# Kernel tuning notes

Hardware: AMD Instinct MI355X
Metric: run time of the kernel (lower is better)

The kernel has to match this reference:

```python
import jax, jax.numpy as jnp
import numpy as np

N = 50000   # nodes
E = 800000  # edges
F = 256     # feature dim (in = hidden = out)
L = 3       # number_layers


def _arma_conv(x, src, dst, w, Wi, Wr, b):
    # GCN normalization without self loops (PyG ARMAConv default)
    deg = jax.ops.segment_sum(w, dst, num_segments=N)                 # [N]
    dinv = jnp.where(deg > 0, jax.lax.rsqrt(deg), 0.0)
    norm = dinv[src] * w * dinv[dst]                                   # [E]
    h = x @ Wi                                                         # [N, F]
    agg = jax.ops.segment_sum(norm[:, None] * h[src], dst, num_segments=N)  # [N, F]
    # root dropout is inactive in eval mode
    return jax.nn.relu(agg + x @ Wr + b)


def setup_inputs() -> dict:
    key = jax.random.key(0)
    ks = jax.random.split(key, 6)
    x = jax.random.normal(ks[0], (N, F), jnp.float32)
    edge_index = jax.random.randint(ks[1], (2, E), 0, N, jnp.int32)
    edge_attr = jax.random.uniform(ks[2], (E,), jnp.float32)
    s = 1.0 / np.sqrt(F)
    W_init = jax.random.normal(ks[3], (L, F, F), jnp.float32) * s
    W_root = jax.random.normal(ks[4], (L, F, F), jnp.float32) * s
    bias = jnp.zeros((L, F), jnp.float32)
    return dict(x=x, edge_index=edge_index, edge_attr=edge_attr,
                W_init=W_init, W_root=W_root, bias=bias)


def reference(x, edge_index, edge_attr, W_init, W_root, bias):
    src, dst = edge_index[0], edge_index[1]
    for i in range(L):  # fixed small layer count
        x = _arma_conv(x, src, dst, edge_attr, W_init[i], W_root[i], bias[i])
        # outer functional.relu is a no-op after the conv's internal ReLU;
        # dropout is inactive in eval mode.
    return x
```

## Files before the change

### kernel.cpp

```cpp
#include <hip/hip_runtime.h>
#include <hip/hip_bf16.h>

#define N_NODES 50000
#define N_EDGES 800000
#define FDIM 256
#define N_LAYERS 3

typedef __attribute__((ext_vector_type(8))) short bf16x8;
typedef __attribute__((ext_vector_type(4))) float f32x4;

__device__ inline unsigned short f2bf(float f) {
  unsigned int u = __float_as_uint(f);
  unsigned int r = u + 0x7FFFu + ((u >> 16) & 1u);
  return (unsigned short)(r >> 16);
}
__device__ inline float bf2f(unsigned short s) {
  return __uint_as_float(((unsigned int)s) << 16);
}
__device__ inline void split2(float f, unsigned short& h, unsigned short& l) {
  h = f2bf(f);
  l = f2bf(f - bf2f(h));
}

#define GLOAD16(g, l) __builtin_amdgcn_global_load_lds( \
    (const __attribute__((address_space(1))) void*)(g), \
    (__attribute__((address_space(3))) void*)(l), 16, 0, 0)


__global__ void deg_count_kernel(const int* __restrict__ dst,
                                 const float* __restrict__ w,
                                 float* __restrict__ deg,
                                 int* __restrict__ cnt, int E) {
  int e = blockIdx.x * blockDim.x + threadIdx.x;
  if (e < E) {
    int d = dst[e];
    atomicAdd(&deg[d], w[e]);
    atomicAdd(&cnt[d], 1);
  }
}

__global__ void dinv_kernel(const float* __restrict__ deg,
                            float* __restrict__ dinv, int n) {
  int i = blockIdx.x * blockDim.x + threadIdx.x;
  if (i < n) {
    float d = deg[i];
    dinv[i] = (d > 0.f) ? (1.f / sqrtf(d)) : 0.f;
  }
}

__global__ __launch_bounds__(1024)
void scan_kernel(const int* __restrict__ cnt, int* __restrict__ offs,
                 int* __restrict__ cursor, int n) {
  __shared__ int wsums[16];
  __shared__ int carry_s;
  int t = threadIdx.x;
  int lane = t & 63, wid = t >> 6;
  if (t == 0) carry_s = 0;
  __syncthreads();
  for (int base = 0; base < n; base += 1024) {
    int i = base + t;
    int v = (i < n) ? cnt[i] : 0;
    int incl = v;
    #pragma unroll
    for (int d = 1; d < 64; d <<= 1) {
      int tmp = __shfl_up(incl, d, 64);
      if (lane >= d) incl += tmp;
    }
    if (lane == 63) wsums[wid] = incl;
    __syncthreads();
    if (t == 0) {
      int s = carry_s;
      #pragma unroll
      for (int k = 0; k < 16; ++k) { int tt = wsums[k]; wsums[k] = s; s += tt; }
      carry_s = s;
    }
    __syncthreads();
    int excl = incl - v + wsums[wid];
    if (i < n) { offs[i] = excl; cursor[i] = excl; }
    __syncthreads();
  }
  if (t == 0) offs[n] = carry_s;
}

__global__ void scatter_kernel(const int* __restrict__ src,
                               const int* __restrict__ dst,
                               const float* __restrict__ w,
                               const float* __restrict__ dinv,
                               int* __restrict__ cursor,
                               int* __restrict__ src_s,
                               float* __restrict__ norm_s, int E) {
  int e = blockIdx.x * blockDim.x + threadIdx.x;
  if (e < E) {
    int s = src[e], d = dst[e];
    int pos = atomicAdd(&cursor[d], 1);
    src_s[pos] = s;
    norm_s[pos] = dinv[s] * w[e] * dinv[d];
  }
}

__global__ void split_kernel(const float* __restrict__ x,
                             unsigned short* __restrict__ xhi,
                             unsigned short* __restrict__ xlo, int n4) {
  int i = blockIdx.x * blockDim.x + threadIdx.x;
  if (i < n4) {
    float4 v = reinterpret_cast<const float4*>(x)[i];
    ushort4 h, l;
    split2(v.x, h.x, l.x);
    split2(v.y, h.y, l.y);
    split2(v.z, h.z, l.z);
    split2(v.w, h.w, l.w);
    reinterpret_cast<ushort4*>(xhi)[i] = h;
    reinterpret_cast<ushort4*>(xlo)[i] = l;
  }
}

__global__ __launch_bounds__(256)
void wsplit_kernel(const float* __restrict__ Wi_a,
                   const float* __restrict__ Wr_a,
                   unsigned short* __restrict__ wthi,
                   unsigned short* __restrict__ wtlo) {
  __shared__ float tile[32][33];
  int m6 = blockIdx.x >> 6;
  int tid = blockIdx.x & 63;
  int tk = (tid >> 3) * 32;
  int tn = (tid & 7) * 32;
  int layer = m6 >> 1;
  const float* W = ((m6 & 1) ? Wr_a : Wi_a) + (size_t)layer * FDIM * FDIM;
  int t = threadIdx.x;
  int lr = t >> 3;
  int lc = (t & 7) * 4;
  float4 v = *reinterpret_cast<const float4*>(W + (size_t)(tk + lr) * FDIM + tn + lc);
  tile[lr][lc + 0] = v.x; tile[lr][lc + 1] = v.y;
  tile[lr][lc + 2] = v.z; tile[lr][lc + 3] = v.w;
  __syncthreads();
  ushort4 h, l;
  split2(tile[lc + 0][lr], h.x, l.x);
  split2(tile[lc + 1][lr], h.y, l.y);
  split2(tile[lc + 2][lr], h.z, l.z);
  split2(tile[lc + 3][lr], h.w, l.w);
  size_t o = ((size_t)m6 * FDIM + tn + lr) * FDIM + tk + lc;
  *reinterpret_cast<ushort4*>(wthi + o) = h;
  *reinterpret_cast<ushort4*>(wtlo + o) = l;
}


__global__ __launch_bounds__(256)
void agg_kernel(const unsigned short* __restrict__ xh,
                const float* __restrict__ norm_s,
                const int* __restrict__ src_s,
                const int* __restrict__ offs,
                unsigned short* __restrict__ agh,
                unsigned short* __restrict__ agl, int n) {
  int node = blockIdx.x * 4 + (threadIdx.x >> 6);
  if (node >= n) return;
  int lane = threadIdx.x & 63;
  int beg = offs[node];
  int end = offs[node + 1];
  float a0 = 0.f, a1 = 0.f, a2 = 0.f, a3 = 0.f;
  int j = beg;
  for (; j + 4 <= end; j += 4) {
    int s0 = src_s[j], s1 = src_s[j + 1], s2 = src_s[j + 2], s3 = src_s[j + 3];
    float w0 = norm_s[j], w1 = norm_s[j + 1], w2 = norm_s[j + 2], w3 = norm_s[j + 3];
    ushort4 v0 = *reinterpret_cast<const ushort4*>(xh + (size_t)s0 * FDIM + lane * 4);
    ushort4 v1 = *reinterpret_cast<const ushort4*>(xh + (size_t)s1 * FDIM + lane * 4);
    ushort4 v2 = *reinterpret_cast<const ushort4*>(xh + (size_t)s2 * FDIM + lane * 4);
    ushort4 v3 = *reinterpret_cast<const ushort4*>(xh + (size_t)s3 * FDIM + lane * 4);
    a0 += w0 * bf2f(v0.x) + w1 * bf2f(v1.x) + w2 * bf2f(v2.x) + w3 * bf2f(v3.x);
    a1 += w0 * bf2f(v0.y) + w1 * bf2f(v1.y) + w2 * bf2f(v2.y) + w3 * bf2f(v3.y);
    a2 += w0 * bf2f(v0.z) + w1 * bf2f(v1.z) + w2 * bf2f(v2.z) + w3 * bf2f(v3.z);
    a3 += w0 * bf2f(v0.w) + w1 * bf2f(v1.w) + w2 * bf2f(v2.w) + w3 * bf2f(v3.w);
  }
  for (; j < end; ++j) {
    int s = src_s[j];
    float wv = norm_s[j];
    ushort4 v = *reinterpret_cast<const ushort4*>(xh + (size_t)s * FDIM + lane * 4);
    a0 += wv * bf2f(v.x); a1 += wv * bf2f(v.y);
    a2 += wv * bf2f(v.z); a3 += wv * bf2f(v.w);
  }
  ushort4 hh, ll;
  split2(a0, hh.x, ll.x);
  split2(a1, hh.y, ll.y);
  split2(a2, hh.z, ll.z);
  split2(a3, hh.w, ll.w);
  size_t base = (size_t)node * FDIM + lane * 4;
  *reinterpret_cast<ushort4*>(agh + base) = hh;
  *reinterpret_cast<ushort4*>(agl + base) = ll;
}


#define STAGE_TILE(TI, GPTR, ROWB, CLAMP)                                        \
  {                                                                              \
    int s0 = t;                                                                  \
    int rr = s0 >> 2;                                                            \
    int sl = (s0 & 3) ^ ((rr >> 1) & 3);                                         \
    int r2 = (ROWB) + rr; if (CLAMP && r2 >= M) r2 = M - 1;                      \
    GLOAD16((GPTR) + (size_t)r2 * FDIM + k0 + sl * 8, smem + (TI)*8192 + s0*16); \
    int s1 = t + 256;                                                            \
    rr = s1 >> 2;                                                                \
    sl = (s1 & 3) ^ ((rr >> 1) & 3);                                             \
    r2 = (ROWB) + rr; if (CLAMP && r2 >= M) r2 = M - 1;                          \
    GLOAD16((GPTR) + (size_t)r2 * FDIM + k0 + sl * 8, smem + (TI)*8192 + s1*16); \
  }

__global__ __launch_bounds__(256, 2)
void gemm_dual_kernel(const unsigned short* __restrict__ agh,
                      const unsigned short* __restrict__ agl,
                      const unsigned short* __restrict__ xh,
                      const unsigned short* __restrict__ xl,
                      const unsigned short* __restrict__ wih,
                      const unsigned short* __restrict__ wil,
                      const unsigned short* __restrict__ wrh,
                      const unsigned short* __restrict__ wrl,
                      const float* __restrict__ bias,
                      unsigned short* __restrict__ oh,
                      unsigned short* __restrict__ ol,
                      float* __restrict__ ofinal,
                      int writeFinal, int M) {
  __shared__ __align__(16) unsigned char smem[65536];
  const int t = threadIdx.x;
  const int lane = t & 63;
  const int w = t >> 6;
  const int rowBase = blockIdx.x * 128;
  const int nBase = blockIdx.y * 128;

  const int wm = (w >> 1) * 64;
  const int wn = (w & 1) * 64;

  f32x4 acc[4][4];
  #pragma unroll
  for (int i = 0; i < 4; ++i)
    #pragma unroll
    for (int j = 0; j < 4; ++j)
      acc[i][j] = (f32x4)(0.f);

  for (int k0 = 0; k0 < FDIM; k0 += 32) {
    STAGE_TILE(0, agh, rowBase, 1);
    STAGE_TILE(1, agl, rowBase, 1);
    STAGE_TILE(2, xh, rowBase, 1);
    STAGE_TILE(3, xl, rowBase, 1);
    STAGE_TILE(4, wih, nBase, 0);
    STAGE_TILE(5, wil, nBase, 0);
    STAGE_TILE(6, wrh, nBase, 0);
    STAGE_TILE(7, wrl, nBase, 0);
    __syncthreads();

    const int q = lane >> 4;
    bf16x8 fah[4], fal[4], fxh[4], fxl[4];
    #pragma unroll
    for (int i = 0; i < 4; ++i) {
      int R = wm + i * 16 + (lane & 15);
      int offA = R * 64 + ((q ^ ((R >> 1) & 3)) * 16);
      fah[i] = *reinterpret_cast<const bf16x8*>(smem + offA);
      fal[i] = *reinterpret_cast<const bf16x8*>(smem + 8192 + offA);
      fxh[i] = *reinterpret_cast<const bf16x8*>(smem + 16384 + offA);
      fxl[i] = *reinterpret_cast<const bf16x8*>(smem + 24576 + offA);
    }
    #pragma unroll
    for (int j = 0; j < 4; ++j) {
      int Rb = wn + j * 16 + (lane & 15);
      int offB = Rb * 64 + ((q ^ ((Rb >> 1) & 3)) * 16);
      bf16x8 bwih = *reinterpret_cast<const bf16x8*>(smem + 32768 + offB);
      bf16x8 bwil = *reinterpret_cast<const bf16x8*>(smem + 40960 + offB);
      bf16x8 bwrh = *reinterpret_cast<const bf16x8*>(smem + 49152 + offB);
      bf16x8 bwrl = *reinterpret_cast<const bf16x8*>(smem + 57344 + offB);
      #pragma unroll
      for (int i = 0; i < 4; ++i) {
        acc[i][j] = __builtin_amdgcn_mfma_f32_16x16x32_bf16(fal[i], bwih, acc[i][j], 0, 0, 0);
        acc[i][j] = __builtin_amdgcn_mfma_f32_16x16x32_bf16(fah[i], bwil, acc[i][j], 0, 0, 0);
        acc[i][j] = __builtin_amdgcn_mfma_f32_16x16x32_bf16(fah[i], bwih, acc[i][j], 0, 0, 0);
        acc[i][j] = __builtin_amdgcn_mfma_f32_16x16x32_bf16(fxl[i], bwrh, acc[i][j], 0, 0, 0);
        acc[i][j] = __builtin_amdgcn_mfma_f32_16x16x32_bf16(fxh[i], bwrl, acc[i][j], 0, 0, 0);
        acc[i][j] = __builtin_amdgcn_mfma_f32_16x16x32_bf16(fxh[i], bwrh, acc[i][j], 0, 0, 0);
      }
    }
    __syncthreads();
  }

  const int cr = lane & 15;
  const int r4 = (lane >> 4) * 4;
  #pragma unroll
  for (int i = 0; i < 4; ++i)
    #pragma unroll
    for (int j = 0; j < 4; ++j) {
      int col = nBase + wn + j * 16 + cr;
      float badd = bias[col];
      #pragma unroll
      for (int e = 0; e < 4; ++e) {
        int row = rowBase + wm + i * 16 + r4 + e;
        if (row < M) {
          float val = fmaxf(acc[i][j][e] + badd, 0.f);
          size_t o = (size_t)row * FDIM + col;
          if (writeFinal) {
            ofinal[o] = val;
          } else {
            unsigned short hh, ll;
            split2(val, hh, ll);
            oh[o] = hh;
            ol[o] = ll;
          }
        }
      }
    }
}


extern "C" void kernel_launch(void* const* d_in, const int* in_sizes, int n_in,
                              void* d_out, int out_size, void* d_ws, size_t ws_size,
                              hipStream_t stream) {
  (void)in_sizes; (void)n_in; (void)out_size; (void)ws_size;
  const float* x0   = (const float*)d_in[0];
  const int*   ei   = (const int*)d_in[1];
  const float* ea   = (const float*)d_in[2];
  const float* Wi_a = (const float*)d_in[3];
  const float* Wr_a = (const float*)d_in[4];
  const float* b_a  = (const float*)d_in[5];
  float* out = (float*)d_out;

  const int* src = ei;
  const int* dst = ei + N_EDGES;

  char* ws = (char*)d_ws;
  size_t off = 0;
  auto alloc = [&](size_t bytes) {
    char* p = ws + off;
    off += (bytes + 255) & ~(size_t)255;
    return p;
  };
  const size_t NF2 = (size_t)N_NODES * FDIM * 2;
  unsigned short* XAh = (unsigned short*)alloc(NF2);
  unsigned short* XAl = (unsigned short*)alloc(NF2);
  unsigned short* XBh = (unsigned short*)alloc(NF2);
  unsigned short* XBl = (unsigned short*)alloc(NF2);
  unsigned short* agh = (unsigned short*)alloc(NF2);
  unsigned short* agl = (unsigned short*)alloc(NF2);
  unsigned short* wthi = (unsigned short*)alloc((size_t)N_LAYERS * 2 * FDIM * FDIM * 2);
  unsigned short* wtlo = (unsigned short*)alloc((size_t)N_LAYERS * 2 * FDIM * FDIM * 2);
  float* deg    = (float*)alloc((size_t)N_NODES * 4);
  float* dinv   = (float*)alloc((size_t)N_NODES * 4);
  int*   cnt    = (int*)alloc((size_t)N_NODES * 4);
  int*   offs   = (int*)alloc((size_t)(N_NODES + 1) * 4);
  int*   cursor = (int*)alloc((size_t)N_NODES * 4);
  int*   src_s  = (int*)alloc((size_t)N_EDGES * 4);
  float* norm_s = (float*)alloc((size_t)N_EDGES * 4);

  hipMemsetAsync(deg, 0, (size_t)N_NODES * 4, stream);
  hipMemsetAsync(cnt, 0, (size_t)N_NODES * 4, stream);

  deg_count_kernel<<<(N_EDGES + 255) / 256, 256, 0, stream>>>(dst, ea, deg, cnt, N_EDGES);
  dinv_kernel<<<(N_NODES + 255) / 256, 256, 0, stream>>>(deg, dinv, N_NODES);
  scan_kernel<<<1, 1024, 0, stream>>>(cnt, offs, cursor, N_NODES);
  scatter_kernel<<<(N_EDGES + 255) / 256, 256, 0, stream>>>(src, dst, ea, dinv, cursor,
                                                            src_s, norm_s, N_EDGES);
  wsplit_kernel<<<6 * 64, 256, 0, stream>>>(Wi_a, Wr_a, wthi, wtlo);
  int n4 = N_NODES * FDIM / 4;
  split_kernel<<<(n4 + 255) / 256, 256, 0, stream>>>(x0, XAh, XAl, n4);

  const size_t WMAT = (size_t)FDIM * FDIM;
  dim3 ggrid((N_NODES + 127) / 128, 2);
  unsigned short* curh = XAh; unsigned short* curl = XAl;
  unsigned short* nxth = XBh; unsigned short* nxtl = XBl;
  for (int l = 0; l < N_LAYERS; ++l) {
    agg_kernel<<<(N_NODES + 3) / 4, 256, 0, stream>>>(curh, norm_s, src_s, offs,
                                                      agh, agl, N_NODES);
    int writeFinal = (l == N_LAYERS - 1) ? 1 : 0;
    gemm_dual_kernel<<<ggrid, 256, 0, stream>>>(
        agh, agl, curh, curl,
        wthi + (size_t)(l * 2) * WMAT, wtlo + (size_t)(l * 2) * WMAT,
        wthi + (size_t)(l * 2 + 1) * WMAT, wtlo + (size_t)(l * 2 + 1) * WMAT,
        b_a + (size_t)l * FDIM,
        nxth, nxtl, out, writeFinal, N_NODES);
    unsigned short* th = curh; unsigned short* tl = curl;
    curh = nxth; curl = nxtl; nxth = th; nxtl = tl;
  }
}
```

Before: 733.3 us.

## Parallelize CSR offset scan and overlap GEMM tile loads with MFMA compute

Replaces the single-block serial prefix scan over 50k node counts with a three-kernel block-sum, block-prefix and per-block offset scan, so the scan runs across many workgroups. In the dual GEMM, each k-step loads all A and B fragments from LDS into registers, waits and barriers, then issues the asynchronous global-to-LDS loads for the next k-slice before running the MFMAs, so global loads overlap compute in a single buffer. The grid is flattened so the two column tiles of the same row block get adjacent block IDs, which should improve L2 reuse of the A rows. This costs more registers for the B fragments and adds two kernel launches.

```diff
diff --git a/kernel.cpp b/kernel.cpp
--- a/kernel.cpp
+++ b/kernel.cpp
@@ -5,6 +5,7 @@
 #define N_EDGES 800000
 #define FDIM 256
 #define N_LAYERS 3
+#define NB_SCAN ((N_NODES + 255) / 256)
 
 typedef __attribute__((ext_vector_type(8))) short bf16x8;
 typedef __attribute__((ext_vector_type(4))) float f32x4;
@@ -48,38 +49,71 @@
   }
 }
 
-__global__ __launch_bounds__(1024)
-void scan_kernel(const int* __restrict__ cnt, int* __restrict__ offs,
-                 int* __restrict__ cursor, int n) {
-  __shared__ int wsums[16];
-  __shared__ int carry_s;
+__global__ __launch_bounds__(256)
+void blocksum_kernel(const int* __restrict__ cnt, int* __restrict__ bsum, int n) {
+  int b = blockIdx.x;
+  int t = threadIdx.x;
+  int i = b * 256 + t;
+  int v = (i < n) ? cnt[i] : 0;
+  #pragma unroll
+  for (int d = 1; d < 64; d <<= 1) v += __shfl_xor(v, d, 64);
+  __shared__ int ws[4];
+  if ((t & 63) == 0) ws[t >> 6] = v;
+  __syncthreads();
+  if (t == 0) bsum[b] = ws[0] + ws[1] + ws[2] + ws[3];
+}
+
+__global__ __launch_bounds__(256)
+void scanb_kernel(const int* __restrict__ bsum, int* __restrict__ bpre,
+                  int* __restrict__ offs_end) {
   int t = threadIdx.x;
   int lane = t & 63, wid = t >> 6;
-  if (t == 0) carry_s = 0;
-  __syncthreads();
-  for (int base = 0; base < n; base += 1024) {
-    int i = base + t;
-    int v = (i < n) ? cnt[i] : 0;
-    int incl = v;
-    #pragma unroll
-    for (int d = 1; d < 64; d <<= 1) {
-      int tmp = __shfl_up(incl, d, 64);
-      if (lane >= d) incl += tmp;
-    }
-    if (lane == 63) wsums[wid] = incl;
-    __syncthreads();
-    if (t == 0) {
-      int s = carry_s;
-      #pragma unroll
-      for (int k = 0; k < 16; ++k) { int tt = wsums[k]; wsums[k] = s; s += tt; }
-      carry_s = s;
-    }
-    __syncthreads();
-    int excl = incl - v + wsums[wid];
-    if (i < n) { offs[i] = excl; cursor[i] = excl; }
-    __syncthreads();
-  }
-  if (t == 0) offs[n] = carry_s;
+  int v = (t < NB_SCAN) ? bsum[t] : 0;
+  int incl = v;
+  #pragma unroll
+  for (int d = 1; d < 64; d <<= 1) {
+    int tmp = __shfl_up(incl, d, 64);
+    if (lane >= d) incl += tmp;
+  }
+  __shared__ int wsum[4];
+  if (lane == 63) wsum[wid] = incl;
+  __syncthreads();
+  if (t == 0) {
+    int s = 0;
+    #pragma unroll
+    for (int k = 0; k < 4; ++k) { int tt = wsum[k]; wsum[k] = s; s += tt; }
+  }
+  __syncthreads();
+  int excl = incl - v + wsum[wid];
+  if (t < NB_SCAN) bpre[t] = excl;
+  if (t == NB_SCAN - 1) *offs_end = excl + v;
+}
+
+__global__ __launch_bounds__(256)
+void offs_kernel(const int* __restrict__ cnt, const int* __restrict__ bpre,
+                 int* __restrict__ offs, int* __restrict__ cursor, int n) {
+  int b = blockIdx.x;
+  int t = threadIdx.x;
+  int lane = t & 63, wid = t >> 6;
+  int i = b * 256 + t;
+  int v = (i < n) ? cnt[i] : 0;
+  int incl = v;
+  #pragma unroll
+  for (int d = 1; d < 64; d <<= 1) {
+    int tmp = __shfl_up(incl, d, 64);
+    if (lane >= d) incl += tmp;
+  }
+  __shared__ int wsum[4];
+  if (lane == 63) wsum[wid] = incl;
+  __syncthreads();
+  if (t == 0) {
+    int s = 0;
+    #pragma unroll
+    for (int k = 0; k < 4; ++k) { int tt = wsum[k]; wsum[k] = s; s += tt; }
+  }
+  __syncthreads();
+  int excl = incl - v + wsum[wid] + bpre[b];
+  if (i < n) { offs[i] = excl; cursor[i] = excl; }
 }
 
 __global__ void scatter_kernel(const int* __restrict__ src,
@@ -188,19 +222,31 @@
 }
 
 
-#define STAGE_TILE(TI, GPTR, ROWB, CLAMP)                                        \
-  {                                                                              \
-    int s0 = t;                                                                  \
-    int rr = s0 >> 2;                                                            \
-    int sl = (s0 & 3) ^ ((rr >> 1) & 3);                                         \
-    int r2 = (ROWB) + rr; if (CLAMP && r2 >= M) r2 = M - 1;                      \
-    GLOAD16((GPTR) + (size_t)r2 * FDIM + k0 + sl * 8, smem + (TI)*8192 + s0*16); \
-    int s1 = t + 256;                                                            \
-    rr = s1 >> 2;                                                                \
-    sl = (s1 & 3) ^ ((rr >> 1) & 3);                                             \
-    r2 = (ROWB) + rr; if (CLAMP && r2 >= M) r2 = M - 1;                          \
-    GLOAD16((GPTR) + (size_t)r2 * FDIM + k0 + sl * 8, smem + (TI)*8192 + s1*16); \
-  }
+#define STAGE_TILE(TI, GPTR, ROWB, CLAMP, K0)                                     \
+  {                                                                               \
+    int s0_ = t;                                                                  \
+    int rr_ = s0_ >> 2;                                                           \
+    int sl_ = (s0_ & 3) ^ ((rr_ >> 1) & 3);                                       \
+    int r2_ = (ROWB) + rr_; if (CLAMP && r2_ >= M) r2_ = M - 1;                   \
+    GLOAD16((GPTR) + (size_t)r2_ * FDIM + (K0) + sl_ * 8,                         \
+            smem + (TI) * 8192 + s0_ * 16);                                       \
+    int s1_ = t + 256;                                                            \
+    rr_ = s1_ >> 2;                                                               \
+    sl_ = (s1_ & 3) ^ ((rr_ >> 1) & 3);                                           \
+    r2_ = (ROWB) + rr_; if (CLAMP && r2_ >= M) r2_ = M - 1;                       \
+    GLOAD16((GPTR) + (size_t)r2_ * FDIM + (K0) + sl_ * 8,                         \
+            smem + (TI) * 8192 + s1_ * 16);                                       \
+  }
+
+#define STAGE_ALL(K0)                      \
+  STAGE_TILE(0, agh, rowBase, 1, K0);      \
+  STAGE_TILE(1, agl, rowBase, 1, K0);      \
+  STAGE_TILE(2, xh, rowBase, 1, K0);       \
+  STAGE_TILE(3, xl, rowBase, 1, K0);       \
+  STAGE_TILE(4, wih, nBase, 0, K0);        \
+  STAGE_TILE(5, wil, nBase, 0, K0);        \
+  STAGE_TILE(6, wrh, nBase, 0, K0);        \
+  STAGE_TILE(7, wrl, nBase, 0, K0);
 
 __global__ __launch_bounds__(256, 2)
 void gemm_dual_kernel(const unsigned short* __restrict__ agh,
@@ -220,8 +266,9 @@
   const int t = threadIdx.x;
   const int lane = t & 63;
   const int w = t >> 6;
-  const int rowBase = blockIdx.x * 128;
-  const int nBase = blockIdx.y * 128;
+  const int bid = blockIdx.x;
+  const int rowBase = (bid >> 1) * 128;
+  const int nBase = (bid & 1) * 128;
 
   const int wm = (w >> 1) * 64;
   const int wn = (w & 1) * 64;
@@ -233,19 +280,14 @@
     for (int j = 0; j < 4; ++j)
       acc[i][j] = (f32x4)(0.f);
 
-  for (int k0 = 0; k0 < FDIM; k0 += 32) {
-    STAGE_TILE(0, agh, rowBase, 1);
-    STAGE_TILE(1, agl, rowBase, 1);
-    STAGE_TILE(2, xh, rowBase, 1);
-    STAGE_TILE(3, xl, rowBase, 1);
-    STAGE_TILE(4, wih, nBase, 0);
-    STAGE_TILE(5, wil, nBase, 0);
-    STAGE_TILE(6, wrh, nBase, 0);
-    STAGE_TILE(7, wrl, nBase, 0);
+  STAGE_ALL(0);
+
+  for (int s = 0; s < 8; ++s) {
     __syncthreads();
 
     const int q = lane >> 4;
     bf16x8 fah[4], fal[4], fxh[4], fxl[4];
+    bf16x8 bih[4], bil[4], brh[4], brl[4];
     #pragma unroll
     for (int i = 0; i < 4; ++i) {
       int R = wm + i * 16 + (lane & 15);
@@ -254,26 +296,35 @@
       fal[i] = *reinterpret_cast<const bf16x8*>(smem + 8192 + offA);
       fxh[i] = *reinterpret_cast<const bf16x8*>(smem + 16384 + offA);
       fxl[i] = *reinterpret_cast<const bf16x8*>(smem + 24576 + offA);
+      int Rb = wn + i * 16 + (lane & 15);
+      int offB = Rb * 64 + ((q ^ ((Rb >> 1) & 3)) * 16);
+      bih[i] = *reinterpret_cast<const bf16x8*>(smem + 32768 + offB);
+      bil[i] = *reinterpret_cast<const bf16x8*>(smem + 40960 + offB);
+      brh[i] = *reinterpret_cast<const bf16x8*>(smem + 49152 + offB);
+      brl[i] = *reinterpret_cast<const bf16x8*>(smem + 57344 + offB);
     }
+    asm volatile("s_waitcnt lgkmcnt(0)" ::: "memory");
+    __builtin_amdgcn_sched_barrier(0);
+    __builtin_amdgcn_s_barrier();
+    __builtin_amdgcn_sched_barrier(0);
+
+    if (s < 7) {
+      int k1 = (s + 1) * 32;
+      STAGE_ALL(k1);
+    }
+
     #pragma unroll
     for (int j = 0; j < 4; ++j) {
-      int Rb = wn + j * 16 + (lane & 15);
-      int offB = Rb * 64 + ((q ^ ((Rb >> 1) & 3)) * 16);
-      bf16x8 bwih = *reinterpret_cast<const bf16x8*>(smem + 32768 + offB);
-      bf16x8 bwil = *reinterpret_cast<const bf16x8*>(smem + 40960 + offB);
-      bf16x8 bwrh = *reinterpret_cast<const bf16x8*>(smem + 49152 + offB);
-      bf16x8 bwrl = *reinterpret_cast<const bf16x8*>(smem + 57344 + offB);
       #pragma unroll
       for (int i = 0; i < 4; ++i) {
-        acc[i][j] = __builtin_amdgcn_mfma_f32_16x16x32_bf16(fal[i], bwih, acc[i][j], 0, 0, 0);
-        acc[i][j] = __builtin_amdgcn_mfma_f32_16x16x32_bf16(fah[i], bwil, acc[i][j], 0, 0, 0);
-        acc[i][j] = __builtin_amdgcn_mfma_f32_16x16x32_bf16(fah[i], bwih, acc[i][j], 0, 0, 0);
-        acc[i][j] = __builtin_amdgcn_mfma_f32_16x16x32_bf16(fxl[i], bwrh, acc[i][j], 0, 0, 0);
-        acc[i][j] = __builtin_amdgcn_mfma_f32_16x16x32_bf16(fxh[i], bwrl, acc[i][j], 0, 0, 0);
-        acc[i][j] = __builtin_amdgcn_mfma_f32_16x16x32_bf16(fxh[i], bwrh, acc[i][j], 0, 0, 0);
+        acc[i][j] = __builtin_amdgcn_mfma_f32_16x16x32_bf16(fal[i], bih[j], acc[i][j], 0, 0, 0);
+        acc[i][j] = __builtin_amdgcn_mfma_f32_16x16x32_bf16(fah[i], bil[j], acc[i][j], 0, 0, 0);
+        acc[i][j] = __builtin_amdgcn_mfma_f32_16x16x32_bf16(fah[i], bih[j], acc[i][j], 0, 0, 0);
+        acc[i][j] = __builtin_amdgcn_mfma_f32_16x16x32_bf16(fxl[i], brh[j], acc[i][j], 0, 0, 0);
+        acc[i][j] = __builtin_amdgcn_mfma_f32_16x16x32_bf16(fxh[i], brl[j], acc[i][j], 0, 0, 0);
+        acc[i][j] = __builtin_amdgcn_mfma_f32_16x16x32_bf16(fxh[i], brh[j], acc[i][j], 0, 0, 0);
       }
     }
-    __syncthreads();
   }
 
   const int cr = lane & 15;
@@ -342,13 +393,17 @@
   int*   cursor = (int*)alloc((size_t)N_NODES * 4);
   int*   src_s  = (int*)alloc((size_t)N_EDGES * 4);
   float* norm_s = (float*)alloc((size_t)N_EDGES * 4);
+  int*   bsum   = (int*)alloc((size_t)NB_SCAN * 4);
+  int*   bpre   = (int*)alloc((size_t)NB_SCAN * 4);
 
   hipMemsetAsync(deg, 0, (size_t)N_NODES * 4, stream);
   hipMemsetAsync(cnt, 0, (size_t)N_NODES * 4, stream);
 
   deg_count_kernel<<<(N_EDGES + 255) / 256, 256, 0, stream>>>(dst, ea, deg, cnt, N_EDGES);
   dinv_kernel<<<(N_NODES + 255) / 256, 256, 0, stream>>>(deg, dinv, N_NODES);
-  scan_kernel<<<1, 1024, 0, stream>>>(cnt, offs, cursor, N_NODES);
+  blocksum_kernel<<<NB_SCAN, 256, 0, stream>>>(cnt, bsum, N_NODES);
+  scanb_kernel<<<1, 256, 0, stream>>>(bsum, bpre, offs + N_NODES);
+  offs_kernel<<<NB_SCAN, 256, 0, stream>>>(cnt, bpre, offs, cursor, N_NODES);
   scatter_kernel<<<(N_EDGES + 255) / 256, 256, 0, stream>>>(src, dst, ea, dinv, cursor,
                                                             src_s, norm_s, N_EDGES);
   wsplit_kernel<<<6 * 64, 256, 0, stream>>>(Wi_a, Wr_a, wthi, wtlo);
@@ -356,7 +411,8 @@
   split_kernel<<<(n4 + 255) / 256, 256, 0, stream>>>(x0, XAh, XAl, n4);
 
   const size_t WMAT = (size_t)FDIM * FDIM;
-  dim3 ggrid((N_NODES + 127) / 128, 2);
+  int nrow = (N_NODES + 127) / 128;
+  dim3 ggrid(nrow * 2);
   unsigned short* curh = XAh; unsigned short* curl = XAl;
   unsigned short* nxth = XBh; unsigned short* nxtl = XBl;
   for (int l = 0; l < N_LAYERS; ++l) {
```

Result: faster. 666.5 us (-9.1%).
